# Optimization experiments

Hardware: AMD Instinct MI355X
Metric: run time of the kernel (lower is better)

Reference implementation:

```python
import jax, jax.numpy as jnp
import numpy as np

IMG_SIZE = 32
PATCH_SIZE = 4
GRID = IMG_SIZE // PATCH_SIZE  # 8 -> 64 patches
EMBED = 768
PATCH_DIM = 1 * 3 * PATCH_SIZE * PATCH_SIZE  # 48
BATCH = 1024


def setup_inputs() -> dict:
    key = jax.random.key(0)
    k1, k2, k3, k4 = jax.random.split(key, 4)
    x = jax.random.normal(k1, (BATCH, 1, 3, IMG_SIZE, IMG_SIZE), dtype=jnp.float32)
    W = jax.random.normal(k2, (EMBED, PATCH_DIM), dtype=jnp.float32) * 0.02  # fc1.weight [out,in]
    cls_token = jax.random.normal(k3, (1, EMBED), dtype=jnp.float32)
    pos_emb = jax.random.normal(k4, (1, GRID * GRID + 1, EMBED), dtype=jnp.float32)
    return {"x": x, "W": W, "cls_token": cls_token, "pos_emb": pos_emb}


def reference(x, W, cls_token, pos_emb):
    B, D1, C, H, Wd = x.shape
    # Row-major patch extraction matching the loop (col fast, row slow).
    # patch flatten order = (D1, C, ph, pw), identical to nn.Flatten(1) on [B,D1,C,P,P].
    patches = x.reshape(B, D1, C, GRID, PATCH_SIZE, GRID, PATCH_SIZE)
    patches = patches.transpose(0, 3, 5, 1, 2, 4, 6)  # [B, gr, gc, D1, C, P, P]
    patches = patches.reshape(B, GRID * GRID, D1 * C * PATCH_SIZE * PATCH_SIZE)  # [B,64,48]
    proj = jnp.einsum('bnp,ep->bne', patches, W)  # fc1 (no bias) -> [B,64,E]
    cls = jnp.broadcast_to(cls_token[None, :, :], (B, 1, EMBED))
    s = jnp.concatenate([cls, proj], axis=1)  # [B,65,E]
    return pos_emb + s
```

## Files before the change

kernel.cpp:

```cpp
#include <hip/hip_runtime.h>


#define BATCH   1024
#define EMBED   768
#define NPATCH  64
#define SEQ     65
#define OUTB    (SEQ * EMBED)

typedef __attribute__((ext_vector_type(8))) short bf16x8;
typedef __attribute__((ext_vector_type(4))) float f32x4;

__device__ __forceinline__ short f2bf(float f) {
    union { float f; unsigned u; } v; v.f = f;
    unsigned r = v.u + 0x7FFFu + ((v.u >> 16) & 1u);
    return (short)(r >> 16);
}

__global__ __launch_bounds__(512, 4) void patch_embed_fused(const float* __restrict__ x,
                                                            const float* __restrict__ W,
                                                            const float* __restrict__ cls,
                                                            const float* __restrict__ pos,
                                                            float* __restrict__ out) {
    __shared__ short A[64 * 64];

    const int tid  = threadIdx.x;
    const int lane = tid & 63;
    const int wave = tid >> 6;
    const int lr   = lane & 15;
    const int lg   = lane >> 4;
    const int ebase = wave * 96;
    const int b = blockIdx.x;

    if (tid < 192) {
        f32x4 cv = ((const f32x4*)cls)[tid];
        f32x4 pv = ((const f32x4*)pos)[tid];
        f32x4 o = cv + pv;
        ((f32x4*)out)[(size_t)b * (OUTB / 4) + tid] = o;
    }

    {
        const int row = tid >> 3;
        const int kb  = tid & 7;
        short* dst = &A[row * 64 + ((kb ^ (row & 7)) * 8)];
        bf16x8 v = {0, 0, 0, 0, 0, 0, 0, 0};
        if (kb < 6) {
            const int c   = kb >> 1;
            const int ph0 = (kb & 1) * 2;
            const int gr = row >> 3, gc = row & 7;
            const float* src = x + (size_t)b * 3072 + c * 1024 + (gr * 4 + ph0) * 32 + gc * 4;
            float4 u0 = *(const float4*)src;
            float4 u1 = *(const float4*)(src + 32);
            v[0] = f2bf(u0.x); v[1] = f2bf(u0.y); v[2] = f2bf(u0.z); v[3] = f2bf(u0.w);
            v[4] = f2bf(u1.x); v[5] = f2bf(u1.y); v[6] = f2bf(u1.z); v[7] = f2bf(u1.w);
        }
        *(bf16x8*)dst = v;
    }

    bf16x8 bw[6][2];
    #pragma unroll
    for (int nt = 0; nt < 6; ++nt) {
        const float* wrow = W + (ebase + nt * 16 + lr) * 48;
        #pragma unroll
        for (int kk = 0; kk < 2; ++kk) {
            const int k0 = kk * 32 + lg * 8;
            bf16x8 f = {0, 0, 0, 0, 0, 0, 0, 0};
            if (k0 < 48) {
                float4 u0 = *(const float4*)(wrow + k0);
                float4 u1 = *(const float4*)(wrow + k0 + 4);
                f[0] = f2bf(u0.x); f[1] = f2bf(u0.y); f[2] = f2bf(u0.z); f[3] = f2bf(u0.w);
                f[4] = f2bf(u1.x); f[5] = f2bf(u1.y); f[6] = f2bf(u1.z); f[7] = f2bf(u1.w);
            }
            bw[nt][kk] = f;
        }
    }

    __syncthreads();

    const size_t outbase = (size_t)b * OUTB + EMBED;
    #pragma unroll 1
    for (int mt = 0; mt < 4; ++mt) {
        const int arow = mt * 16 + lr;
        const int sw0  = ((0 * 4 + lg) ^ (arow & 7)) * 8;
        const int sw1  = ((1 * 4 + lg) ^ (arow & 7)) * 8;
        bf16x8 a0 = *(const bf16x8*)&A[arow * 64 + sw0];
        bf16x8 a1 = *(const bf16x8*)&A[arow * 64 + sw1];

        f32x4 acc[6];
        const f32x4 zero = {0.f, 0.f, 0.f, 0.f};
        #pragma unroll
        for (int nt = 0; nt < 6; ++nt)
            acc[nt] = __builtin_amdgcn_mfma_f32_16x16x32_bf16(a0, bw[nt][0], zero, 0, 0, 0);
        #pragma unroll
        for (int nt = 0; nt < 6; ++nt)
            acc[nt] = __builtin_amdgcn_mfma_f32_16x16x32_bf16(a1, bw[nt][1], acc[nt], 0, 0, 0);

        #pragma unroll
        for (int j = 0; j < 4; ++j) {
            const int n = mt * 16 + lg * 4 + j;
            const float* prow = pos + (size_t)(n + 1) * EMBED + ebase + lr;
            float* orow = out + outbase + (size_t)n * EMBED + ebase + lr;
            #pragma unroll
            for (int nt = 0; nt < 6; ++nt)
                orow[nt * 16] = acc[nt][j] + prow[nt * 16];
        }
    }
}

extern "C" void kernel_launch(void* const* d_in, const int* in_sizes, int n_in,
                              void* d_out, int out_size, void* d_ws, size_t ws_size,
                              hipStream_t stream) {
    const float* x   = (const float*)d_in[0];
    const float* W   = (const float*)d_in[1];
    const float* cls = (const float*)d_in[2];
    const float* pos = (const float*)d_in[3];
    float* out = (float*)d_out;

    hipLaunchKernelGGL(patch_embed_fused, dim3(BATCH), dim3(512), 0, stream,
                       x, W, cls, pos, out);
}
```

Before: 46.77 us.

## Split into prep kernel for bf16 weights and finer-grained main GEMM blocks

Adds a prep kernel that converts W to bf16 once into workspace and writes the cls rows. The main kernel now uses 8 blocks per batch (one 16-patch tile and half the embed dim each) with 256 threads, and loads pre-converted bf16 weights directly. This removes the per-block fp32-to-bf16 weight conversion and increases parallelism. In exchange it adds a second launch, and each block loads its weights for only a single MFMA tile, so weight reuse per block drops.

```diff
diff --git a/kernel.cpp b/kernel.cpp
--- a/kernel.cpp
+++ b/kernel.cpp
@@ -6,6 +6,7 @@
 #define NPATCH  64
 #define SEQ     65
 #define OUTB    (SEQ * EMBED)
+#define WELEMS  (EMBED * 48)
 
 typedef __attribute__((ext_vector_type(8))) short bf16x8;
 typedef __attribute__((ext_vector_type(4))) float f32x4;
@@ -16,37 +17,59 @@
     return (short)(r >> 16);
 }
 
-__global__ __launch_bounds__(512, 4) void patch_embed_fused(const float* __restrict__ x,
-                                                            const float* __restrict__ W,
-                                                            const float* __restrict__ cls,
-                                                            const float* __restrict__ pos,
-                                                            float* __restrict__ out) {
-    __shared__ short A[64 * 64];
+__global__ __launch_bounds__(256) void prep_kernel(const float* __restrict__ W,
+                                                   const float* __restrict__ cls,
+                                                   const float* __restrict__ pos,
+                                                   short* __restrict__ w16,
+                                                   float* __restrict__ out) {
+    const int tid = threadIdx.x;
+    const int bid = blockIdx.x;
+    if (bid < 18) {
+        const int i = (bid * 256 + tid) * 8;
+        float4 u0 = *(const float4*)(W + i);
+        float4 u1 = *(const float4*)(W + i + 4);
+        bf16x8 v;
+        v[0] = f2bf(u0.x); v[1] = f2bf(u0.y); v[2] = f2bf(u0.z); v[3] = f2bf(u0.w);
+        v[4] = f2bf(u1.x); v[5] = f2bf(u1.y); v[6] = f2bf(u1.z); v[7] = f2bf(u1.w);
+        *(bf16x8*)(w16 + i) = v;
+    } else {
+        const int b = bid - 18;
+        if (tid < 192) {
+            f32x4 cv = ((const f32x4*)cls)[tid];
+            f32x4 pv = ((const f32x4*)pos)[tid];
+            ((f32x4*)out)[(size_t)b * (OUTB / 4) + tid] = cv + pv;
+        }
+    }
+}
+
+__global__ __launch_bounds__(256, 4) void patch_embed_main(const float* __restrict__ x,
+                                                           const short* __restrict__ w16,
+                                                           const float* __restrict__ pos,
+                                                           float* __restrict__ out) {
+    __shared__ short A[16 * 64];
 
     const int tid  = threadIdx.x;
     const int lane = tid & 63;
     const int wave = tid >> 6;
     const int lr   = lane & 15;
     const int lg   = lane >> 4;
-    const int ebase = wave * 96;
-    const int b = blockIdx.x;
+    const int bid  = blockIdx.x;
+    const int b    = bid >> 3;
+    const int sub  = bid & 7;
+    const int mt   = sub >> 1;
+    const int eh   = sub & 1;
+    const int ebase = eh * 384 + wave * 96;
 
-    if (tid < 192) {
-        f32x4 cv = ((const f32x4*)cls)[tid];
-        f32x4 pv = ((const f32x4*)pos)[tid];
-        f32x4 o = cv + pv;
-        ((f32x4*)out)[(size_t)b * (OUTB / 4) + tid] = o;
-    }
-
-    {
+    if (tid < 128) {
         const int row = tid >> 3;
         const int kb  = tid & 7;
         short* dst = &A[row * 64 + ((kb ^ (row & 7)) * 8)];
         bf16x8 v = {0, 0, 0, 0, 0, 0, 0, 0};
         if (kb < 6) {
+            const int n   = mt * 16 + row;
             const int c   = kb >> 1;
             const int ph0 = (kb & 1) * 2;
-            const int gr = row >> 3, gc = row & 7;
+            const int gr = n >> 3, gc = n & 7;
             const float* src = x + (size_t)b * 3072 + c * 1024 + (gr * 4 + ph0) * 32 + gc * 4;
             float4 u0 = *(const float4*)src;
             float4 u1 = *(const float4*)(src + 32);
@@ -59,50 +82,36 @@
     bf16x8 bw[6][2];
     #pragma unroll
     for (int nt = 0; nt < 6; ++nt) {
-        const float* wrow = W + (ebase + nt * 16 + lr) * 48;
-        #pragma unroll
-        for (int kk = 0; kk < 2; ++kk) {
-            const int k0 = kk * 32 + lg * 8;
-            bf16x8 f = {0, 0, 0, 0, 0, 0, 0, 0};
-            if (k0 < 48) {
-                float4 u0 = *(const float4*)(wrow + k0);
-                float4 u1 = *(const float4*)(wrow + k0 + 4);
-                f[0] = f2bf(u0.x); f[1] = f2bf(u0.y); f[2] = f2bf(u0.z); f[3] = f2bf(u0.w);
-                f[4] = f2bf(u1.x); f[5] = f2bf(u1.y); f[6] = f2bf(u1.z); f[7] = f2bf(u1.w);
-            }
-            bw[nt][kk] = f;
-        }
+        const short* wrow = w16 + (ebase + nt * 16 + lr) * 48;
+        bw[nt][0] = *(const bf16x8*)(wrow + lg * 8);
+        const int k1 = 32 + lg * 8;
+        bf16x8 f = {0, 0, 0, 0, 0, 0, 0, 0};
+        if (k1 < 48) f = *(const bf16x8*)(wrow + k1);
+        bw[nt][1] = f;
     }
 
     __syncthreads();
 
-    const size_t outbase = (size_t)b * OUTB + EMBED;
-    #pragma unroll 1
-    for (int mt = 0; mt < 4; ++mt) {
-        const int arow = mt * 16 + lr;
-        const int sw0  = ((0 * 4 + lg) ^ (arow & 7)) * 8;
-        const int sw1  = ((1 * 4 + lg) ^ (arow & 7)) * 8;
-        bf16x8 a0 = *(const bf16x8*)&A[arow * 64 + sw0];
-        bf16x8 a1 = *(const bf16x8*)&A[arow * 64 + sw1];
+    bf16x8 a0 = *(const bf16x8*)&A[lr * 64 + ((lg ^ (lr & 7)) * 8)];
+    bf16x8 a1 = *(const bf16x8*)&A[lr * 64 + (((4 + lg) ^ (lr & 7)) * 8)];
 
-        f32x4 acc[6];
-        const f32x4 zero = {0.f, 0.f, 0.f, 0.f};
+    f32x4 acc[6];
+    const f32x4 zero = {0.f, 0.f, 0.f, 0.f};
+    #pragma unroll
+    for (int nt = 0; nt < 6; ++nt)
+        acc[nt] = __builtin_amdgcn_mfma_f32_16x16x32_bf16(a0, bw[nt][0], zero, 0, 0, 0);
+    #pragma unroll
+    for (int nt = 0; nt < 6; ++nt)
+        acc[nt] = __builtin_amdgcn_mfma_f32_16x16x32_bf16(a1, bw[nt][1], acc[nt], 0, 0, 0);
+
+    #pragma unroll
+    for (int j = 0; j < 4; ++j) {
+        const int n = mt * 16 + lg * 4 + j;
+        const float* prow = pos + (size_t)(n + 1) * EMBED + ebase + lr;
+        float* orow = out + (size_t)b * OUTB + (size_t)(n + 1) * EMBED + ebase + lr;
         #pragma unroll
         for (int nt = 0; nt < 6; ++nt)
-            acc[nt] = __builtin_amdgcn_mfma_f32_16x16x32_bf16(a0, bw[nt][0], zero, 0, 0, 0);
-        #pragma unroll
-        for (int nt = 0; nt < 6; ++nt)
-            acc[nt] = __builtin_amdgcn_mfma_f32_16x16x32_bf16(a1, bw[nt][1], acc[nt], 0, 0, 0);
-
-        #pragma unroll
-        for (int j = 0; j < 4; ++j) {
-            const int n = mt * 16 + lg * 4 + j;
-            const float* prow = pos + (size_t)(n + 1) * EMBED + ebase + lr;
-            float* orow = out + outbase + (size_t)n * EMBED + ebase + lr;
-            #pragma unroll
-            for (int nt = 0; nt < 6; ++nt)
-                orow[nt * 16] = acc[nt][j] + prow[nt * 16];
-        }
+            orow[nt * 16] = acc[nt][j] + prow[nt * 16];
     }
 }
 
@@ -114,7 +123,10 @@
     const float* cls = (const float*)d_in[2];
     const float* pos = (const float*)d_in[3];
     float* out = (float*)d_out;
+    short* w16 = (short*)d_ws;
 
-    hipLaunchKernelGGL(patch_embed_fused, dim3(BATCH), dim3(512), 0, stream,
-                       x, W, cls, pos, out);
+    hipLaunchKernelGGL(prep_kernel, dim3(18 + BATCH), dim3(256), 0, stream,
+                       W, cls, pos, w16, out);
+    hipLaunchKernelGGL(patch_embed_main, dim3(BATCH * 8), dim3(256), 0, stream,
+                       x, w16, pos, out);
 }
```

Result: no change. 47.69 us (+2.0%).
